# Optimization experiments

Hardware: AMD Instinct MI355X
Metric: run time of the kernel (lower is better)

## Reference

```python
import jax, jax.numpy as jnp
import numpy as np

WINDOW_3D = (5, 11, 11)
SIGMA_3D = (0.7, 1.5, 1.5)
VALUE_MAGNITUDE = 1.0
USE_GAUSSIAN = True
CHANNEL = 1


def _gaussian(n, sigma):
    x = np.arange(n, dtype=np.float64)
    g = np.exp(-((x - n // 2) ** 2) / (2.0 * sigma ** 2))
    return g / g.sum()


def _make_window():
    if USE_GAUSSIAN:
        wz = _gaussian(WINDOW_3D[0], SIGMA_3D[0])
        wy = _gaussian(WINDOW_3D[1], SIGMA_3D[1])
        wx = _gaussian(WINDOW_3D[2], SIGMA_3D[2])
    else:
        wz = np.full(WINDOW_3D[0], 1.0 / WINDOW_3D[0])
        wy = np.full(WINDOW_3D[1], 1.0 / WINDOW_3D[1])
        wx = np.full(WINDOW_3D[2], 1.0 / WINDOW_3D[2])
    win = np.einsum('z,y,x->zyx', wz, wy, wx).astype(np.float32)
    # depthwise kernel: (C, 1, wz, wy, wx)
    return jnp.asarray(np.broadcast_to(win, (CHANNEL, 1) + WINDOW_3D).copy())


def _dwconv3d(x, w):
    pad = [(s // 2, s // 2) for s in WINDOW_3D]
    return jax.lax.conv_general_dilated(
        x, w, window_strides=(1, 1, 1), padding=pad,
        dimension_numbers=('NCDHW', 'OIDHW', 'NCDHW'),
        feature_group_count=CHANNEL)


def setup_inputs() -> dict:
    key = jax.random.key(0)
    k1, k2 = jax.random.split(key)
    shape = (8, 1, 32, 256, 256)
    img1 = jax.random.uniform(k1, shape, dtype=jnp.float32)
    img2 = jax.random.uniform(k2, shape, dtype=jnp.float32)
    return {"img1": img1, "img2": img2}


def reference(img1, img2):
    w = _make_window().astype(img1.dtype)
    mu1 = _dwconv3d(img1, w)
    mu2 = _dwconv3d(img2, w)
    mu1_sq = mu1 * mu1
    mu2_sq = mu2 * mu2
    mu1_mu2 = mu1 * mu2
    sigma1_sq = _dwconv3d(img1 * img1, w) - mu1_sq
    sigma2_sq = _dwconv3d(img2 * img2, w) - mu2_sq
    sigma12 = _dwconv3d(img1 * img2, w) - mu1_mu2
    C1 = (VALUE_MAGNITUDE * 0.01) ** 2
    C2 = (VALUE_MAGNITUDE * 0.03) ** 2
    ssim_map = ((2 * mu1_mu2 + C1) * (2 * sigma12 + C2)) / (
        (mu1_sq + mu2_sq + C1) * (sigma1_sq + sigma2_sq + C2))
    ssim = jnp.mean(ssim_map, axis=(0, 2, 3, 4))  # per-channel mean
    return 1.0 - ssim
```

## Files before the change

kernel.cpp:

```cpp
#include <hip/hip_runtime.h>


typedef __attribute__((ext_vector_type(2))) float f32x2;
typedef _Float16 h2 __attribute__((ext_vector_type(2)));

#define DEPTH   32
#define HEIGHT  256
#define WIDTH   256
#define HW      (HEIGHT*WIDTH)
#define COUNT   16777216.0
#define NACC    64
#define NF      4

#define PDW   23
#define PLSZ  (44*PDW)

#define W0h 0x1436u
#define W1h 0x1FC8u
#define W2h 0x289Cu
#define W3h 0x2F00u
#define W4h 0x32D1u
#define W5h 0x3442u

__device__ __forceinline__ h2 h2bits(unsigned u) {
  h2 r; __builtin_memcpy(&r, &u, 4); return r;
}
__device__ __forceinline__ h2 hfma2v(h2 a, h2 b, h2 c) {
  return __builtin_elementwise_fma(a, b, c);
}
__device__ __forceinline__ h2 pkrtz(float x, float y) {
#if __has_builtin(__builtin_amdgcn_cvt_pkrtz)
  auto t = __builtin_amdgcn_cvt_pkrtz(x, y);
  h2 r; __builtin_memcpy(&r, &t, 4); return r;
#else
  h2 r; r.x = (_Float16)x; r.y = (_Float16)y; return r;
#endif
}

__global__ __launch_bounds__(256, 6) void ssim3d_h16e(
    const float* __restrict__ img1, const float* __restrict__ img2,
    double* __restrict__ acc)
{
  __shared__ __align__(16) h2 PL[NF * PLSZ];
  __shared__ float wred[4];
  const int tid = threadIdx.x;

  constexpr unsigned WYB[11] = {
    W0h|(W0h<<16), W1h|(W1h<<16), W2h|(W2h<<16), W3h|(W3h<<16), W4h|(W4h<<16),
    W5h|(W5h<<16),
    W4h|(W4h<<16), W3h|(W3h<<16), W2h|(W2h<<16), W1h|(W1h<<16), W0h|(W0h<<16)};
  constexpr unsigned WZB[5] = {
    0x20ED20EDu, 0x32933293u, 0x388F388Fu, 0x32933293u, 0x20ED20EDu};
  constexpr unsigned WP[4][8] = {
    {0x14360000u, 0x289C1FC8u, 0x32D12F00u, 0x32D13442u, 0x289C2F00u, 0x14361FC8u, 0u, 0u},
    {0u, 0x1FC81436u, 0x2F00289Cu, 0x344232D1u, 0x2F0032D1u, 0x1FC8289Cu, 0x00001436u, 0u},
    {0u, 0x14360000u, 0x289C1FC8u, 0x32D12F00u, 0x32D13442u, 0x289C2F00u, 0x14361FC8u, 0u},
    {0u, 0u, 0x1FC81436u, 0x2F00289Cu, 0x344232D1u, 0x2F0032D1u, 0x1FC8289Cu, 0x00001436u}};

  int bid = blockIdx.x;
  bid = (bid & 7) * 2048 + (bid >> 3);
  const int txi = bid & 7, tyi = (bid >> 3) & 7, z_out = (bid >> 6) & 31, n = bid >> 11;
  const int x0 = txi * 32 - 6;
  const int y0 = tyi * 32 - 5;

  const int cp = tid % 22, g = tid / 22;
  h2 zacc[4][NF];
#pragma unroll
  for (int i = 0; i < 4; ++i)
#pragma unroll
    for (int f = 0; f < NF; ++f) zacc[i][f] = (h2){(_Float16)0, (_Float16)0};

  if (g < 11) {
    const int gx0 = x0 + 2 * cp;
    if ((unsigned)gx0 <= 254u) {
      const size_t nbase = (size_t)n * DEPTH * HW;
      int rofs[4];
#pragma unroll
      for (int i = 0; i < 4; ++i) {
        int gy = y0 + 4 * g + i;
        rofs[i] = min(max(gy, 0), 255) * WIDTH;
      }
#pragma unroll
      for (int kz = 0; kz < 5; ++kz) {
        int z_in = z_out + kz - 2;
        if ((unsigned)z_in >= 32u) continue;
        const h2 wzh = h2bits(WZB[kz]);
        const float* p1 = img1 + nbase + (size_t)z_in * HW + gx0;
        const float* p2 = img2 + nbase + (size_t)z_in * HW + gx0;
#pragma unroll
        for (int i = 0; i < 4; ++i) {
          f32x2 A = *(const f32x2*)(p1 + rofs[i]);
          f32x2 B = *(const f32x2*)(p2 + rofs[i]);
          h2 ah = pkrtz(A.x, A.y), bh = pkrtz(B.x, B.y);
          h2 ss = hfma2v(ah, ah, bh * bh);
          zacc[i][0] = hfma2v(wzh, ah, zacc[i][0]);
          zacc[i][1] = hfma2v(wzh, bh, zacc[i][1]);
          zacc[i][2] = hfma2v(wzh, ss, zacc[i][2]);
          zacc[i][3] = hfma2v(wzh, ah * bh, zacc[i][3]);
        }
      }
    }
#pragma unroll
    for (int i = 0; i < 4; ++i) {
      int row = 4 * g + i;
#pragma unroll
      for (int f = 0; f < NF; ++f)
        PL[f * PLSZ + row * PDW + cp] = zacc[i][f];
    }
  }
  __syncthreads();

  const int g2 = tid / 22, xp = tid % 22;
  const bool act3 = (g2 < 11);
  const bool yedge = (tyi == 0) || (tyi == 7);
#pragma unroll
  for (int f = 0; f < NF; ++f) {
    h2 yout[3];
    if (act3) {
      const h2* pf = PL + f * PLSZ + xp;
      h2 win[13];
#pragma unroll
      for (int i = 0; i < 13; ++i) win[i] = pf[(3 * g2 + i) * PDW];
      if (yedge) {
#pragma unroll
        for (int i = 0; i < 13; ++i)
          if ((unsigned)(y0 + 3 * g2 + i) >= 256u)
            win[i] = (h2){(_Float16)0, (_Float16)0};
      }
#pragma unroll
      for (int r = 0; r < 3; ++r) {
        h2 s = (h2){(_Float16)0, (_Float16)0};
#pragma unroll
        for (int j = 0; j < 11; ++j) s = hfma2v(h2bits(WYB[j]), win[r + j], s);
        yout[r] = s;
      }
    }
    __syncthreads();
    if (act3) {
#pragma unroll
      for (int r = 0; r < 3; ++r) {
        int y = 3 * g2 + r;
        if (y < 32) PL[f * PLSZ + y * PDW + xp] = yout[r];
      }
    }
  }
  __syncthreads();

  const int yy = tid & 31;
  const int xh = tid >> 5;
  float sf[NF][4];
#pragma unroll
  for (int f = 0; f < NF; ++f) {
    const h2* pp = PL + f * PLSZ + yy * PDW + xh * 2;
    h2 d[8];
#pragma unroll
    for (int m = 0; m < 8; ++m) d[m] = pp[m];
#pragma unroll
    for (int k = 0; k < 4; ++k) {
      h2 a = (h2){(_Float16)0, (_Float16)0};
#pragma unroll
      for (int m = 0; m < 8; ++m)
        if (WP[k][m]) a = hfma2v(h2bits(WP[k][m]), d[m], a);
      sf[f][k] = (float)a.x + (float)a.y;
    }
  }

  float lsum = 0.f;
  const float C1 = 1e-4f, C2 = 9e-4f;
#pragma unroll
  for (int k = 0; k < 4; ++k) {
    float mu1 = sf[0][k], mu2 = sf[1][k];
    float mps = fmaf(mu1, mu1, mu2 * mu2);
    float m12 = mu1 * mu2;
    float s12 = sf[3][k] - m12;
    float sps = sf[2][k] - mps;
    float num = fmaf(2.f, m12, C1) * fmaf(2.f, s12, C2);
    float den = (mps + C1) * (sps + C2);
#if __has_builtin(__builtin_amdgcn_rcpf)
    lsum = fmaf(num, __builtin_amdgcn_rcpf(den), lsum);
#else
    lsum += num / den;
#endif
  }

#pragma unroll
  for (int off = 32; off > 0; off >>= 1) lsum += __shfl_down(lsum, off, 64);
  if ((tid & 63) == 0) wred[tid >> 6] = lsum;
  __syncthreads();
  if (tid == 0) {
    float bs = wred[0] + wred[1] + wred[2] + wred[3];
    atomicAdd(&acc[blockIdx.x & (NACC - 1)], (double)bs);
  }
}

__global__ void ssim3d_finalize(const double* __restrict__ acc, float* __restrict__ out)
{
  double s = 0.0;
  for (int i = 0; i < NACC; ++i) s += acc[i];
  out[0] = 1.0f - (float)(s / COUNT);
}

extern "C" void kernel_launch(void* const* d_in, const int* in_sizes, int n_in,
                              void* d_out, int out_size, void* d_ws, size_t ws_size,
                              hipStream_t stream)
{
  const float* img1 = (const float*)d_in[0];
  const float* img2 = (const float*)d_in[1];
  float* out = (float*)d_out;
  double* acc = (double*)d_ws;

  (void)hipMemsetAsync(d_ws, 0, NACC * sizeof(double), stream);

  const int n_blocks = 8 * DEPTH * 8 * 8;
  ssim3d_h16e<<<dim3(n_blocks), dim3(256), 0, stream>>>(img1, img2, acc);
  ssim3d_finalize<<<1, 1, 0, stream>>>(acc, out);
}
```

Before: 108.8 us.

## Make y- and x-pass wave-private to drop block barriers and shared reduction

Each wavefront now computes the y-direction conv for its own 8 output rows (4 rows per lane, 44 active lanes), writes them to a wave-private LDS buffer and immediately runs the x-pass from it. This removes the per-field __syncthreads and the in-place overwrite of PL. Wave synchronisation relies only on an lgkmcnt wait. The block-level reduction through shared memory is replaced by one double atomic per wave spread over the accumulators. The cost is extra LDS (the PRIV buffer), some redundant window loads, and four times as many atomics.

```diff
diff --git a/kernel.cpp b/kernel.cpp
--- a/kernel.cpp
+++ b/kernel.cpp
@@ -14,6 +14,8 @@
 
 #define PDW   23
 #define PLSZ  (44*PDW)
+#define PRSTR 23
+#define PRSZ  (8*PRSTR)
 
 #define W0h 0x1436u
 #define W1h 0x1FC8u
@@ -37,12 +39,12 @@
 #endif
 }
 
-__global__ __launch_bounds__(256, 6) void ssim3d_h16e(
+__global__ __launch_bounds__(256, 6) void ssim3d_wv2(
     const float* __restrict__ img1, const float* __restrict__ img2,
     double* __restrict__ acc)
 {
   __shared__ __align__(16) h2 PL[NF * PLSZ];
-  __shared__ float wred[4];
+  __shared__ __align__(16) h2 PRIV[4 * PRSZ];
   const int tid = threadIdx.x;
 
   constexpr unsigned WYB[11] = {
@@ -110,59 +112,54 @@
   }
   __syncthreads();
 
-  const int g2 = tid / 22, xp = tid % 22;
-  const bool act3 = (g2 < 11);
+  const int wv = tid >> 6, lane = tid & 63;
+  const int rbase = wv << 3;
+  const int c3 = lane % 22, h3 = lane / 22;
+  const bool a3 = (h3 < 2);
+  const int r3 = rbase + 4 * h3;
+  const int r4 = lane >> 3, q4 = lane & 7;
+  h2* pb = PRIV + wv * PRSZ;
   const bool yedge = (tyi == 0) || (tyi == 7);
+
+  float sf[NF][4];
 #pragma unroll
   for (int f = 0; f < NF; ++f) {
-    h2 yout[3];
-    if (act3) {
-      const h2* pf = PL + f * PLSZ + xp;
-      h2 win[13];
-#pragma unroll
-      for (int i = 0; i < 13; ++i) win[i] = pf[(3 * g2 + i) * PDW];
+    if (a3) {
+      const h2* pf = PL + f * PLSZ + c3;
+      h2 win[14];
+#pragma unroll
+      for (int i = 0; i < 14; ++i) win[i] = pf[(r3 + i) * PDW];
       if (yedge) {
 #pragma unroll
-        for (int i = 0; i < 13; ++i)
-          if ((unsigned)(y0 + 3 * g2 + i) >= 256u)
+        for (int i = 0; i < 14; ++i)
+          if ((unsigned)(y0 + r3 + i) >= 256u)
             win[i] = (h2){(_Float16)0, (_Float16)0};
       }
 #pragma unroll
-      for (int r = 0; r < 3; ++r) {
+      for (int r = 0; r < 4; ++r) {
         h2 s = (h2){(_Float16)0, (_Float16)0};
 #pragma unroll
         for (int j = 0; j < 11; ++j) s = hfma2v(h2bits(WYB[j]), win[r + j], s);
-        yout[r] = s;
-      }
-    }
-    __syncthreads();
-    if (act3) {
-#pragma unroll
-      for (int r = 0; r < 3; ++r) {
-        int y = 3 * g2 + r;
-        if (y < 32) PL[f * PLSZ + y * PDW + xp] = yout[r];
-      }
-    }
-  }
-  __syncthreads();
-
-  const int yy = tid & 31;
-  const int xh = tid >> 5;
-  float sf[NF][4];
-#pragma unroll
-  for (int f = 0; f < NF; ++f) {
-    const h2* pp = PL + f * PLSZ + yy * PDW + xh * 2;
-    h2 d[8];
-#pragma unroll
-    for (int m = 0; m < 8; ++m) d[m] = pp[m];
-#pragma unroll
-    for (int k = 0; k < 4; ++k) {
-      h2 a = (h2){(_Float16)0, (_Float16)0};
-#pragma unroll
-      for (int m = 0; m < 8; ++m)
-        if (WP[k][m]) a = hfma2v(h2bits(WP[k][m]), d[m], a);
-      sf[f][k] = (float)a.x + (float)a.y;
-    }
+        pb[(4 * h3 + r) * PRSTR + c3] = s;
+      }
+    }
+    asm volatile("s_waitcnt lgkmcnt(0)" ::: "memory");
+
+    {
+      const h2* pp = pb + r4 * PRSTR + q4 * 2;
+      h2 d[8];
+#pragma unroll
+      for (int m = 0; m < 8; ++m) d[m] = pp[m];
+#pragma unroll
+      for (int k = 0; k < 4; ++k) {
+        h2 a = (h2){(_Float16)0, (_Float16)0};
+#pragma unroll
+        for (int m = 0; m < 8; ++m)
+          if (WP[k][m]) a = hfma2v(h2bits(WP[k][m]), d[m], a);
+        sf[f][k] = (float)a.x + (float)a.y;
+      }
+    }
+    asm volatile("" ::: "memory");
   }
 
   float lsum = 0.f;
@@ -185,12 +182,8 @@
 
 #pragma unroll
   for (int off = 32; off > 0; off >>= 1) lsum += __shfl_down(lsum, off, 64);
-  if ((tid & 63) == 0) wred[tid >> 6] = lsum;
-  __syncthreads();
-  if (tid == 0) {
-    float bs = wred[0] + wred[1] + wred[2] + wred[3];
-    atomicAdd(&acc[blockIdx.x & (NACC - 1)], (double)bs);
-  }
+  if (lane == 0)
+    atomicAdd(&acc[(blockIdx.x * 4 + wv) & (NACC - 1)], (double)lsum);
 }
 
 __global__ void ssim3d_finalize(const double* __restrict__ acc, float* __restrict__ out)
@@ -212,6 +205,6 @@
   (void)hipMemsetAsync(d_ws, 0, NACC * sizeof(double), stream);
 
   const int n_blocks = 8 * DEPTH * 8 * 8;
-  ssim3d_h16e<<<dim3(n_blocks), dim3(256), 0, stream>>>(img1, img2, acc);
+  ssim3d_wv2<<<dim3(n_blocks), dim3(256), 0, stream>>>(img1, img2, acc);
   ssim3d_finalize<<<1, 1, 0, stream>>>(acc, out);
 }
```

After: 203.9 us. 1.87x slower.
